# Optimization experiments

Measured on AMD Instinct MI355X. Metric: run time of the kernel, lower is better.

The kernel has to match this reference:

```python
import jax, jax.numpy as jnp
import numpy as np

MOLS = 64
ATOMS = 256
N = MOLS * ATOMS
K_GB = 32
K_GNN = 16
HID = 128
OFFSET = 0.009            # GB dielectric offset (nm)
ALPHA, BETA, GAMMA = 1.0, 0.8, 4.85  # OBC2 coefficients
EPS_FACTOR = 138.935456   # Coulomb constant, kJ*nm/(mol*e^2)
PREF = -EPS_FACTOR * (1.0 - 1.0 / 78.5)


def _edges(key, k_neigh):
    # random intra-molecule neighbors, no self loops (mimics radius-graph structure)
    src = jnp.repeat(jnp.arange(N), k_neigh)
    off = jax.random.randint(key, (N * k_neigh,), 1, ATOMS)
    dst = (src // ATOMS) * ATOMS + (src % ATOMS + off) % ATOMS
    return jnp.stack([src, dst]).astype(jnp.int32)


def setup_inputs() -> dict:
    key = jax.random.key(0)
    ks = jax.random.split(key, 8)
    pos = (jax.random.uniform(ks[0], (N, 3), jnp.float32) * 1.5)
    q = jax.random.uniform(ks[1], (N, 1), jnp.float32) - 0.5
    rad = 0.15 + 0.05 * jax.random.uniform(ks[2], (N, 1), jnp.float32)
    scl = 0.8 + 0.2 * jax.random.uniform(ks[3], (N, 1), jnp.float32)
    rest = jax.random.uniform(ks[4], (N, 4), jnp.float32)
    atom_features = jnp.concatenate([q, rad, scl, rest], axis=1)
    batch = jnp.repeat(jnp.arange(MOLS), ATOMS).astype(jnp.int32)
    edge_index = _edges(ks[5], K_GB)
    gnn_edge_index = _edges(ks[6], K_GNN)

    def lin(k, fi, fo):
        return (jax.random.normal(k, (fi, fo), jnp.float32) / np.float32(np.sqrt(fi)),
                jnp.zeros((fo,), jnp.float32))
    kw = jax.random.split(ks[7], 6)
    i1_w1, i1_b1 = lin(kw[0], 2 * 2 + 1, HID)
    i1_w2, i1_b2 = lin(kw[1], HID, HID)
    i2_w1, i2_b1 = lin(kw[2], 2 * HID + 1, HID)
    i2_w2, i2_b2 = lin(kw[3], HID, HID)
    i3_w1, i3_b1 = lin(kw[4], 2 * HID + 1, HID)
    i3_w2, i3_b2 = lin(kw[5], HID, 1)
    return dict(pos=pos, atom_features=atom_features, batch=batch,
                edge_index=edge_index, gnn_edge_index=gnn_edge_index,
                i1_w1=i1_w1, i1_b1=i1_b1, i1_w2=i1_w2, i1_b2=i1_b2,
                i2_w1=i2_w1, i2_b1=i2_b1, i2_w2=i2_w2, i2_b2=i2_b2,
                i3_w1=i3_w1, i3_b1=i3_b1, i3_w2=i3_w2, i3_b2=i3_b2)


def _dist(pos, ei):
    d2 = jnp.sum((pos[ei[0]] - pos[ei[1]]) ** 2, axis=1)
    return jnp.sqrt(d2 + 1e-12)


def _gb_energies(pos, feats, ei):
    # GBNeck_interaction (Born radii via HCT descreening integral, OBC2 rescale)
    # followed by GBNeck_energies (pairwise GB + self energy), per-atom [N,1]
    n = pos.shape[0]
    src, dst = ei[0], ei[1]
    d = _dist(pos, ei)
    q, radius, scale = feats[:, 0], feats[:, 1], feats[:, 2]
    rho = radius - OFFSET
    sr_j = (scale * rho)[src]
    rho_i = rho[dst]
    U = d + sr_j
    L = jnp.maximum(rho_i, jnp.abs(d - sr_j))
    I = 0.5 * (1.0 / L - 1.0 / U
               + 0.25 * (d - sr_j ** 2 / d) * (1.0 / U ** 2 - 1.0 / L ** 2)
               + 0.5 * jnp.log(L / U) / d)
    I = jnp.where(rho_i < U, I, 0.0)
    Isum = jax.ops.segment_sum(I, dst, num_segments=n)
    psi = Isum * rho
    B = 1.0 / (1.0 / rho - jnp.tanh(ALPHA * psi - BETA * psi ** 2 + GAMMA * psi ** 3) / radius)
    Bi, Bj = B[dst], B[src]
    f_gb = jnp.sqrt(d ** 2 + Bi * Bj * jnp.exp(-d ** 2 / (4.0 * Bi * Bj)))
    e_pair = 0.5 * PREF * q[dst] * q[src] / f_gb  # 0.5: edges are double counted
    e = 0.5 * PREF * q ** 2 / B + jax.ops.segment_sum(e_pair, dst, num_segments=n)
    return e[:, None]


def _in_layer(x, ei, d, w1, b1, w2, b2):
    # IN_layer_all_swish_2pass: edge MLP on [x_i || x_j || d] + scatter-add
    n = x.shape[0]
    m = jnp.concatenate([x[ei[0]], x[ei[1]], d[:, None]], axis=1)
    h = jax.nn.silu(m @ w1 + b1)
    return jax.ops.segment_sum(h @ w2 + b2, ei[1], num_segments=n)


def _energies_all(pos, feats, ei, gei,
                  i1_w1, i1_b1, i1_w2, i1_b2,
                  i2_w1, i2_b1, i2_w2, i2_b2,
                  i3_w1, i3_b1, i3_w2, i3_b2):
    e_gb = _gb_energies(pos, feats, ei)
    d_gnn = _dist(pos, gei)
    x = jax.nn.silu(_in_layer(feats[:, :2], gei, d_gnn, i1_w1, i1_b1, i1_w2, i1_b2))
    x = jax.nn.silu(_in_layer(x, gei, d_gnn, i2_w1, i2_b1, i2_w2, i2_b2))
    x = _in_layer(x, gei, d_gnn, i3_w1, i3_b1, i3_w2, i3_b2)
    return e_gb + x


def reference(pos, atom_features, batch, edge_index, gnn_edge_index,
              i1_w1, i1_b1, i1_w2, i1_b2,
              i2_w1, i2_b1, i2_w2, i2_b2,
              i3_w1, i3_b1, i3_w2, i3_b2):
    ws = (i1_w1, i1_b1, i1_w2, i1_b2, i2_w1, i2_b1, i2_w2, i2_b2,
          i3_w1, i3_b1, i3_w2, i3_b2)
    efun = lambda p: _energies_all(p, atom_features, edge_index, gnn_edge_index, *ws)
    energies, vjp = jax.vjp(efun, pos)  # [N,1]
    (gpos,) = vjp(jnp.ones_like(energies))
    forces = -gpos
    energy = jax.ops.segment_sum(energies[:, 0], batch, num_segments=MOLS)[:, None]
    return energy, forces
```

## Files before the change

kernel.cpp:

```cpp
#include <hip/hip_runtime.h>
#include <hip/hip_bf16.h>

#define NATOMS 16384
#define MOLS   64
#define ATOMSM 256
#define EGB    524288
#define EGNN   262144
#define HID    128
#define NH     (NATOMS*HID)

#define OFFSETC 0.009f
#define ALPHAC  1.0f
#define BETAC   0.8f
#define GAMMAC  4.85f
#define PREFC   (-138.935456f*(1.0f-1.0f/78.5f))

typedef __hip_bfloat16 bf;
typedef __attribute__((ext_vector_type(8))) short bf8v;
typedef __attribute__((ext_vector_type(4))) float f4v;
typedef unsigned int uint;

__device__ __forceinline__ float b2f(bf x){ return __bfloat162float(x); }
__device__ __forceinline__ bf f2b(float x){ return __float2bfloat16(x); }
__device__ __forceinline__ short f2s(float x){ bf h = f2b(x); return *(short*)&h; }
// ... 53 lines not shown
    short* __restrict__ A3at, short* __restrict__ A3bt,
    short* __restrict__ rA2a, short* __restrict__ rA2b,
    short* __restrict__ rA3a, short* __restrict__ rA3b,
    short* __restrict__ rC1, short* __restrict__ rC2,
    const float* __restrict__ feat, const float* __restrict__ A1,
    bf* __restrict__ u1, bf* __restrict__ v1,
    const float* __restrict__ pos, const int* __restrict__ ei,
    float* __restrict__ Isum,
    const int* __restrict__ gei, float* __restrict__ dgnn, int* __restrict__ cnt)
{
    int tid = threadIdx.x;
    if (blockIdx.x < 64){
        int gid = blockIdx.x*256 + tid;
        int j = gid >> 7, k = gid & 127;
        C1t[gid]  = f2s(C1[k*HID+j]);
        C2t[gid]  = f2s(C2[k*HID+j]);
        A2at[gid] = f2s(A2[k*HID+j]);
        A2bt[gid] = f2s(A2[(HID+k)*HID+j]);
        A3at[gid] = f2s(A3[k*HID+j]);
        A3bt[gid] = f2s(A3[(HID+k)*HID+j]);
        rA2a[gid] = f2s(A2[gid]);
        rA2b[gid] = f2s(A2[HID*HID+gid]);
        rA3a[gid] = f2s(A3[gid]);
        rA3b[gid] = f2s(A3[HID*HID+gid]);
        rC1[gid]  = f2s(C1[gid]);
        rC2[gid]  = f2s(C2[gid]);
    } else if (blockIdx.x < 4160){
        int gid2 = (blockIdx.x-64)*256 + tid;
        int i = gid2 >> 6, k2 = (gid2 & 63)*2;
        float q = feat[7*i+0], r = feat[7*i+1];
        float u0 = q*A1[k2]         + r*A1[HID+k2];
        float u1v= q*A1[k2+1]       + r*A1[HID+k2+1];
        float v0 = q*A1[2*HID+k2]   + r*A1[3*HID+k2];
        float v1v= q*A1[2*HID+k2+1] + r*A1[3*HID+k2+1];
        ushort2 uu, vv;
        uu.x = (unsigned short)f2s(u0); uu.y = (unsigned short)f2s(u1v);
        vv.x = (unsigned short)f2s(v0); vv.y = (unsigned short)f2s(v1v);
        *(ushort2*)((short*)u1 + (size_t)i*HID + k2) = uu;
        *(ushort2*)((short*)v1 + (size_t)i*HID + k2) = vv;
    } else if (blockIdx.x < 4672){
        __shared__ float sPx[256], sPy[256], sPz[256], sRho[256], sSr[256];
        __shared__ float sI[256];
        int bb = blockIdx.x - 4160;
        int mbase = (bb >> 3) * 256;
        {
            int i = mbase + tid;
            sPx[tid]=pos[3*i]; sPy[tid]=pos[3*i+1]; sPz[tid]=pos[3*i+2];
            float rad = feat[7*i+1], sc = feat[7*i+2];
            float rho = rad - OFFSETC;
            sRho[tid]=rho; sSr[tid]=sc*rho;
            sI[tid]=0.f;
        }
        __syncthreads();
        int T = bb*256 + tid;
        int s = T >> 3, p = T & 7;
        int sl = s & 255;
        int e0 = s*32 + p*4;
        float px = sPx[sl], py = sPy[sl], pz = sPz[sl];
        float sr = sSr[sl];
        float srr = sr*sr;
        const int* dP = ei + EGB;
        int4 d4 = *(const int4*)(dP + e0);
        int dls[4] = {d4.x&255, d4.y&255, d4.z&255, d4.w&255};
#pragma unroll
        for (int j=0;j<4;j++){
            int dl = dls[j];
            float dx = px - sPx[dl];
            float dy = py - sPy[dl];
            float dz = pz - sPz[dl];
            float d2 = dx*dx+dy*dy+dz*dz + 1e-12f;
            float rd = frsq(d2);
            float d  = d2*rd;
            float rho_i = sRho[dl];
            float U = d + sr;
            if (rho_i < U){
                float L = fmaxf(rho_i, fabsf(d - sr));
                float invU = frcp(U), invL = frcp(L);
                float I = 0.5f*invL - 0.5f*invU
                        + 0.125f*(d - srr*rd)*(invU*invU - invL*invL)
                        + 0.25f*__logf(L*invU)*rd;
                atomicAdd(&sI[dl], I);
            }
        }
        __syncthreads();
        atomicAdd(&Isum[mbase + tid], sI[tid]);
    } else {
        int e = (blockIdx.x-4672)*256 + tid;
        int s = gei[e], dd = gei[EGNN+e];
        float dx = pos[3*s+0] - pos[3*dd+0];
        float dy = pos[3*s+1] - pos[3*dd+1];
        float dz = pos[3*s+2] - pos[3*dd+2];
        dgnn[e] = fsqrt(dx*dx+dy*dy+dz*dz + 1e-12f);
        atomicAdd(&cnt[dd], 1);
    }
}

__global__ __launch_bounds__(256) void k_B(
    const float* __restrict__ feat, const float* __restrict__ Isum,
    float* __restrict__ Bv, float* __restrict__ cB, float* __restrict__ gB,
    float* __restrict__ egb,
    const int* __restrict__ cnt, int* __restrict__ rptr,
    const int* __restrict__ gei, const float* __restrict__ dgnn,
    int* __restrict__ csr, int2* __restrict__ csr2)
{
    int t = threadIdx.x;
    if (blockIdx.x < 64){
        int i = blockIdx.x*256 + t;
        float q   = feat[7*i+0];
        float rad = feat[7*i+1];
        float rho = rad - OFFSETC;
        float psi = Isum[i]*rho;
        float u = psi*(ALPHAC + psi*(-BETAC + GAMMAC*psi));
        float tt = tanhf(u);
        float rrad = frcp(rad);
        float B = frcp(frcp(rho) - tt*rrad);
        Bv[i] = B;
        float du = ALPHAC + psi*(-2.0f*BETAC + 3.0f*GAMMAC*psi);
        cB[i] = B*B*((1.0f-tt*tt)*rrad)*du*rho;
        float Cs = 0.5f*PREFC*q*q;
        float rB = frcp(B);
        egb[i] = Cs*rB;
        gB[i]  = -Cs*rB*rB;
    } else {
        __shared__ int sc[256];
        __shared__ int lcur[256];
        int m = blockIdx.x - 64;
        int c = cnt[m*256+t];
        sc[t] = c; __syncthreads();
        for (int off=1; off<256; off<<=1){
            int x = (t>=off) ? sc[t-off] : 0;
            __syncthreads();
            sc[t] += x;
            __syncthreads();
        }
        int exl = sc[t] - c;
        rptr[m*256+t] = m*4096 + exl;
        lcur[t] = exl;
        __syncthreads();
        int e0 = m*4096;
        for (int j=t; j<4096; j+=256){
            int e = e0 + j;
            int dl = gei[EGNN+e] & 255;
            float d = dgnn[e];
            int p = atomicAdd(&lcur[dl], 1);
            int idx = e0 + p;
            csr[idx] = e;
            int2 rec; rec.x = (e >> 4) << 8;
            rec.y = __float_as_int(d);
            csr2[idx] = rec;
        }
    }
}

__global__ __launch_bounds__(256) void k_gbC(
    const float* __restrict__ pos, const float* __restrict__ feat,
    const int* __restrict__ ei, const float* __restrict__ Bv,
    float* __restrict__ egb, float* __restrict__ gdgb, float* __restrict__ gB)
{
    __shared__ float sPx[256], sPy[256], sPz[256], sB[256], sQf[256];
    __shared__ float sE[256], sG[256];
    int tid = threadIdx.x;
    int mbase = (blockIdx.x >> 3) * 256;
    {
        int i = mbase + tid;
        sPx[tid]=pos[3*i]; sPy[tid]=pos[3*i+1]; sPz[tid]=pos[3*i+2];
        sB[tid]=Bv[i]; sQf[tid]=feat[7*i+0];
        sE[tid]=0.f; sG[tid]=0.f;
    }
    __syncthreads();
    int T = blockIdx.x*256 + tid;
    int s = T >> 3, p = T & 7;
    int sl = s & 255;
    int e0 = s*32 + p*4;
    float px = sPx[sl], py = sPy[sl], pz = sPz[sl];
    float qs = sQf[sl];
    float Bs = sB[sl];
    float gsrc = 0.f;
    const int* dP = ei + EGB;
    int4 d4 = *(const int4*)(dP + e0);
    int dls[4] = {d4.x&255, d4.y&255, d4.z&255, d4.w&255};
#pragma unroll
    for (int j=0;j<4;j++){
        int dl = dls[j];
        float dx = px - sPx[dl];
        float dy = py - sPy[dl];
        float dz = pz - sPz[dl];
        float d2 = dx*dx+dy*dy+dz*dz + 1e-12f;
        float d  = d2*frsq(d2);
        float Bd = sB[dl];
        float C = 0.5f*PREFC*sQf[dl]*qs;
        float P = Bd*Bs;
        float qq = 0.25f*d2*frcp(P);
        float ex = __expf(-qq);
        float f2 = d2 + P*ex;
        float rf = frsq(f2);
        float f3i = rf*rf*rf;
        gdgb[e0+j] = -C*d*(1.f - 0.25f*ex)*f3i;
        float common = -C*ex*(1.f + qq)*0.5f*f3i;
        atomicAdd(&sE[dl], C*rf);
        atomicAdd(&sG[dl], common*Bs);
        gsrc += common*Bd;
    }
    gsrc += __shfl_xor(gsrc,1);
    gsrc += __shfl_xor(gsrc,2);
    gsrc += __shfl_xor(gsrc,4);
    if (p==0) atomicAdd(&sG[sl], gsrc);
    __syncthreads();
    atomicAdd(&egb[mbase + tid], sE[tid]);
    atomicAdd(&gB[mbase + tid],  sG[tid]);
}

__global__ __launch_bounds__(256) void k_gbE(
    const float* __restrict__ pos, const float* __restrict__ feat,
    const int* __restrict__ ei, const float* __restrict__ cB,
    const float* __restrict__ gB,
    const float* __restrict__ gdgb, float* __restrict__ grad)
{
    __shared__ float sPx[256], sPy[256], sPz[256], sRho[256], sSr[256], sCg[256];
    __shared__ float sGx[256], sGy[256], sGz[256];
    int tid = threadIdx.x;
    int mbase = (blockIdx.x >> 3) * 256;
    {
        int i = mbase + tid;
        sPx[tid]=pos[3*i]; sPy[tid]=pos[3*i+1]; sPz[tid]=pos[3*i+2];
        float rad = feat[7*i+1], sc = feat[7*i+2];
        float rho = rad - OFFSETC;
        sRho[tid]=rho; sSr[tid]=sc*rho;
        sCg[tid]=cB[i]*gB[i];
        sGx[tid]=0.f; sGy[tid]=0.f; sGz[tid]=0.f;
    }
    __syncthreads();
    int T = blockIdx.x*256 + tid;
    int s = T >> 3, p = T & 7;
    int sl = s & 255;
    int e0 = s*32 + p*4;
    float px = sPx[sl], py = sPy[sl], pz = sPz[sl];
    float sr = sSr[sl];
    float srr = sr*sr;
    float gx=0.f, gy=0.f, gz=0.f;
    const int* dP = ei + EGB;
    int4 d4 = *(const int4*)(dP + e0);
    int dls[4] = {d4.x&255, d4.y&255, d4.z&255, d4.w&255};
#pragma unroll
    for (int j=0;j<4;j++){
        int dl = dls[j];
        float dx = px - sPx[dl];
        float dy = py - sPy[dl];
        float dz = pz - sPz[dl];
        float d2 = dx*dx+dy*dy+dz*dz + 1e-12f;
        float rd = frsq(d2);
        float d  = d2*rd;
        float rd2 = rd*rd;
        float rho_i = sRho[dl];
        float U = d + sr;
        float gd = gdgb[e0+j];
        if (rho_i < U){
            float aa = fabsf(d - sr);
            float L, Lp;
            if (rho_i >= aa){ L = rho_i; Lp = 0.f; }
            else { L = aa; Lp = (d >= sr) ? 1.f : -1.f; }
            float invU = frcp(U), invL = frcp(L);
            float invU2=invU*invU, invL2=invL*invL;
            float dIdd = -0.5f*Lp*invL2 + 0.5f*invU2
                + 0.125f*(1.f + srr*rd2)*(invU2 - invL2)
                + 0.125f*(d - srr*rd)*(2.f*Lp*invL2*invL - 2.f*invU2*invU)
                + 0.25f*((Lp*invL - invU)*rd - __logf(L*invU)*rd2);
            gd += sCg[dl]*dIdd;
        }
        float c = gd*rd;
        gx += c*dx; gy += c*dy; gz += c*dz;
        atomicAdd(&sGx[dl], -c*dx);
        atomicAdd(&sGy[dl], -c*dy);
        atomicAdd(&sGz[dl], -c*dz);
    }
    gx += __shfl_xor(gx,1); gx += __shfl_xor(gx,2); gx += __shfl_xor(gx,4);
    gy += __shfl_xor(gy,1); gy += __shfl_xor(gy,2); gy += __shfl_xor(gy,4);
    gz += __shfl_xor(gz,1); gz += __shfl_xor(gz,2); gz += __shfl_xor(gz,4);
    if (p==0){
        atomicAdd(&sGx[sl], gx);
        atomicAdd(&sGy[sl], gy);
        atomicAdd(&sGz[sl], gz);
    }
    __syncthreads();
    int i = mbase + tid;
    atomicAdd(&grad[3*i+0], sGx[tid]);
    atomicAdd(&grad[3*i+1], sGy[tid]);
    atomicAdd(&grad[3*i+2], sGz[tid]);
}


template<bool WSDS>
__device__ __forceinline__ void edge_fwd_wave(
    int dst, int lane,
    const int2* __restrict__ csr2, const int* __restrict__ rptr, const int* __restrict__ cnt,
    const uint* __restrict__ u, const uint* __restrict__ v,
    const float* __restrict__ wdp, const float* __restrict__ bb,
    uint* __restrict__ Hs, uint* __restrict__ Sds)
{
    int n = cnt[dst], r0 = rptr[dst];
    float2 wd = *(const float2*)&wdp[2*lane];
    float2 b2 = *(const float2*)&bb[2*lane];
    uint vp = v[dst*64 + lane];
    float base0 = lo2f(vp) + b2.x;
    float base1 = hi2f(vp) + b2.y;
    float h0=0.f,h1=0.f,e0a=0.f,e1a=0.f;
    for (int j0=0; j0<n; j0+=64){
        int m = n - j0; if (m > 64) m = 64;
        int rx = 0, ry = 0;
        if (lane < m){ int2 rc = csr2[r0+j0+lane]; rx = rc.x; ry = rc.y; }
#pragma unroll 2
        for (int j=0;j<m;j++){
            int off = __builtin_amdgcn_readlane(rx, j);
            float d  = __uint_as_float((unsigned)__builtin_amdgcn_readlane(ry, j));
            uint up = *(const uint*)((const char*)u + off + 4*lane);
            float a0 = fmaf(d, wd.x, base0 + lo2f(up));
            float a1 = fmaf(d, wd.y, base1 + hi2f(up));
            float s0 = sigf(a0), s1 = sigf(a1);
            float p0 = a0*s0, p1 = a1*s1;
            h0 += p0; h1 += p1;
            if (WSDS){
                e0a = fmaf(s0, 1.f + a0 - p0, e0a);
                e1a = fmaf(s1, 1.f + a1 - p1, e1a);
            }
        }
    }
    Hs[dst*64+lane] = pack2(h0,h1);
    if (WSDS) Sds[dst*64+lane] = pack2(e0a,e1a);
}

__global__ __launch_bounds__(256,8) void k_edge_fwd0(
    const int2* __restrict__ csr2, const int* __restrict__ rptr, const int* __restrict__ cnt,
    const uint* __restrict__ u, const uint* __restrict__ v,
    const float* __restrict__ wdp, const float* __restrict__ bb,
    uint* __restrict__ Hs)
{
    int lane = threadIdx.x & 63, wid = threadIdx.x >> 6;
    int dst = blockIdx.x*4 + wid;
    edge_fwd_wave<false>(dst, lane, csr2, rptr, cnt, u, v, wdp, bb, Hs, nullptr);
}

__global__ __launch_bounds__(256,8) void k_edge_fwd1(
    const int2* __restrict__ csr2, const int* __restrict__ rptr, const int* __restrict__ cnt,
    const uint* __restrict__ u, const uint* __restrict__ v,
    const float* __restrict__ wdp, const float* __restrict__ bb,
    uint* __restrict__ Hs, uint* __restrict__ Sds)
{
    int lane = threadIdx.x & 63, wid = threadIdx.x >> 6;
    int dst = blockIdx.x*4 + wid;
    edge_fwd_wave<true>(dst, lane, csr2, rptr, cnt, u, v, wdp, bb, Hs, Sds);
}

__global__ __launch_bounds__(256,4) void k_l3(
    const int2* __restrict__ csr2, const int* __restrict__ rptr, const int* __restrict__ cnt,
    const int* __restrict__ gei, const float* __restrict__ dgnn,
    const uint* __restrict__ u, const uint* __restrict__ v,
    const float* __restrict__ A3, const float* __restrict__ B3,
    const float* __restrict__ C3, const float* __restrict__ D3,
    uint* __restrict__ Gd, float* __restrict__ x3,
    uint* __restrict__ Gs, float* __restrict__ gdg)
{
    int lane = threadIdx.x & 63, wid = threadIdx.x >> 6;
    const float* wdp = A3 + 256*HID;
    if (blockIdx.x < NATOMS/4){
        int dst = blockIdx.x*4 + wid;
        int n = cnt[dst], r0 = rptr[dst];
        float2 wd = *(const float2*)&wdp[2*lane];
        float2 b2 = *(const float2*)&B3[2*lane];
        float2 ck = *(const float2*)&C3[2*lane];
        uint vp = v[dst*64 + lane];
        float base0 = lo2f(vp) + b2.x;
        float base1 = hi2f(vp) + b2.y;
        float h0=0.f,h1=0.f,e0a=0.f,e1a=0.f;
        for (int j0=0; j0<n; j0+=64){
            int m = n - j0; if (m > 64) m = 64;
            int rx = 0, ry = 0;
            if (lane < m){ int2 rc = csr2[r0+j0+lane]; rx = rc.x; ry = rc.y; }
#pragma unroll 2
            for (int j=0;j<m;j++){
                int off = __builtin_amdgcn_readlane(rx, j);
                float d  = __uint_as_float((unsigned)__builtin_amdgcn_readlane(ry, j));
                uint up = *(const uint*)((const char*)u + off + 4*lane);
                float a0 = fmaf(d, wd.x, base0 + lo2f(up));
                float a1 = fmaf(d, wd.y, base1 + hi2f(up));
                float s0 = sigf(a0), s1 = sigf(a1);
                float p0 = a0*s0, p1 = a1*s1;
                h0 += p0; h1 += p1;
                e0a = fmaf(s0, 1.f + a0 - p0, e0a);
                e1a = fmaf(s1, 1.f + a1 - p1, e1a);
            }
        }
        Gd[dst*64+lane] = pack2(ck.x*e0a, ck.y*e1a);
        float px = waveRed(ck.x*h0 + ck.y*h1);
        if (lane==0) x3[dst] = px + (float)n*D3[0];
    } else {
        int s = (blockIdx.x - NATOMS/4)*4 + wid;
        int doff = 0, dbit = 0;
        if (lane < 16){
            doff = gei[EGNN + s*16 + lane] << 8;
            dbit = __float_as_int(dgnn[s*16+lane]);
        }
        float2 wd = *(const float2*)&wdp[2*lane];
        float2 b2 = *(const float2*)&B3[2*lane];
        float2 ck = *(const float2*)&C3[2*lane];
        uint up = u[s*64 + lane];
        float us0 = lo2f(up) + b2.x;
        float us1 = hi2f(up) + b2.y;
        float cw0 = ck.x*wd.x, cw1 = ck.y*wd.y;
        float gs0=0.f, gs1=0.f;
        float A[16];
#pragma unroll
        for (int t=0;t<16;t++){
            int off = __builtin_amdgcn_readlane(doff, t);
            float d = __uint_as_float((unsigned)__builtin_amdgcn_readlane(dbit, t));
            uint vp = *(const uint*)((const char*)v + off + 4*lane);
            float a0 = fmaf(d, wd.x, us0 + lo2f(vp));
            float a1 = fmaf(d, wd.y, us1 + hi2f(vp));
            float s0 = sigf(a0), s1 = sigf(a1);
            float p0 = a0*s0, p1 = a1*s1;
            float dv0 = s0*(1.f + a0 - p0);
            float dv1 = s1*(1.f + a1 - p1);
            gs0 += dv0; gs1 += dv1;
            A[t] = fmaf(dv1, cw1, dv0*cw0);
        }
        Gs[s*64+lane] = pack2(ck.x*gs0, ck.y*gs1);
        float tot = red16(A, lane);
        if (lane < 32 && !(lane & 1)) gdg[s*16 + (lane>>1)] = tot;
    }
}

__global__ __launch_bounds__(256,4) void k_bwd_src(
    const int* __restrict__ gei, const float* __restrict__ dgnn,
    const uint* __restrict__ u, const uint* __restrict__ v,
    const float* __restrict__ wdp, const float* __restrict__ bb,
    const uint* __restrict__ gH,
    uint* __restrict__ Gs, float* __restrict__ gdg)
{
    int lane = threadIdx.x & 63, wid = threadIdx.x >> 6;
    int s = blockIdx.x*4 + wid;
    int doff = 0, dbit = 0;
    if (lane < 16){
        doff = gei[EGNN + s*16 + lane] << 8;
        dbit = __float_as_int(dgnn[s*16+lane]);
    }
    float gold = gdg[s*16 + ((lane>>1)&15)];
    float2 wd = *(const float2*)&wdp[2*lane];
    float2 b2 = *(const float2*)&bb[2*lane];
    uint up = u[s*64 + lane];
    float us0 = lo2f(up) + b2.x;
    float us1 = hi2f(up) + b2.y;
    float gs0=0.f, gs1=0.f;
    float A[16];
#pragma unroll
    for (int t=0;t<16;t++){
        int off = __builtin_amdgcn_readlane(doff, t);
        float d = __uint_as_float((unsigned)__builtin_amdgcn_readlane(dbit, t));
        uint vp = *(const uint*)((const char*)v + off + 4*lane);
        uint gp = *(const uint*)((const char*)gH + off + 4*lane);
        float a0 = fmaf(d, wd.x, us0 + lo2f(vp));
        float a1 = fmaf(d, wd.y, us1 + hi2f(vp));
        float s0 = sigf(a0), s1 = sigf(a1);
        float p0 = a0*s0, p1 = a1*s1;
        float ga0 = s0*(1.f + a0 - p0) * lo2f(gp);
        float ga1 = s1*(1.f + a1 - p1) * hi2f(gp);
        gs0 += ga0; gs1 += ga1;
        A[t] = fmaf(ga1, wd.y, ga0*wd.x);
    }
    if (Gs) Gs[s*64+lane] = pack2(gs0, gs1);
    float tot = red16(A, lane);
    if (lane < 32 && !(lane & 1)) gdg[s*16 + (lane>>1)] = gold + tot;
}

__global__ __launch_bounds__(256) void k_node_fwd_uv_mfma(
    const short* __restrict__ Hs, const int* __restrict__ cnt,
    const short* __restrict__ Ct, const float* __restrict__ D,
    const short* __restrict__ Aat, const short* __restrict__ Abt,
    bf* __restrict__ dsz, bf* __restrict__ u, bf* __restrict__ v)
{
    __shared__ short sx[64*HID];
    int lane = threadIdx.x & 63, w = threadIdx.x >> 6;
    int m0 = blockIdx.x*64 + w*16;
    int ar = lane & 15, kg = lane >> 4;
    bf8v af[4];
#pragma unroll
    for (int s=0;s<4;s++) af[s] = *(const bf8v*)&Hs[(size_t)(m0+ar)*HID + s*32 + kg*8];
    f4v acc[8];
#pragma unroll
    for (int nt=0;nt<8;nt++){
        acc[nt] = (f4v){0.f,0.f,0.f,0.f};
        const short* bp = Ct + (nt*16+ar)*HID + kg*8;
#pragma unroll
        for (int s=0;s<4;s++){
            bf8v bv = *(const bf8v*)(bp + s*32);
            acc[nt] = __builtin_amdgcn_mfma_f32_16x16x32_bf16(af[s], bv, acc[nt], 0,0,0);
        }
    }
    float cn[4];
#pragma unroll
    for (int r=0;r<4;r++) cn[r] = (float)cnt[m0 + kg*4 + r];
#pragma unroll
    for (int nt=0;nt<8;nt++){
        int j = nt*16 + ar;
        float Dj = D[j];
#pragma unroll
        for (int r=0;r<4;r++){
            int m = m0 + kg*4 + r;
            float zv = acc[nt][r] + cn[r]*Dj;
            float sg = sigf(zv);
            dsz[(size_t)m*HID + j] = f2b(sg*(1.f + zv*(1.f - sg)));
            sx[(w*16 + kg*4 + r)*HID + j] = f2s(zv*sg);
        }
    }
    __syncthreads();
#pragma unroll
    for (int s=0;s<4;s++) af[s] = *(const bf8v*)&sx[(w*16+ar)*HID + s*32 + kg*8];
    f4v au[8], av[8];
#pragma unroll
    for (int nt=0;nt<8;nt++){
        au[nt] = (f4v){0.f,0.f,0.f,0.f};
        av[nt] = (f4v){0.f,0.f,0.f,0.f};
        const short* bpa = Aat + (nt*16+ar)*HID + kg*8;
        const short* bpb = Abt + (nt*16+ar)*HID + kg*8;
#pragma unroll
        for (int s=0;s<4;s++){
            bf8v ba = *(const bf8v*)(bpa + s*32);
            bf8v bb = *(const bf8v*)(bpb + s*32);
            au[nt] = __builtin_amdgcn_mfma_f32_16x16x32_bf16(af[s], ba, au[nt], 0,0,0);
            av[nt] = __builtin_amdgcn_mfma_f32_16x16x32_bf16(af[s], bb, av[nt], 0,0,0);
        }
    }
#pragma unroll
    for (int nt=0;nt<8;nt++){
        int j = nt*16 + ar;
#pragma unroll
        for (int r=0;r<4;r++){
            int m = m0 + kg*4 + r;
            u[(size_t)m*HID + j] = f2b(au[nt][r]);
            v[(size_t)m*HID + j] = f2b(av[nt][r]);
        }
    }
}

__global__ __launch_bounds__(256) void k_gx_node_bwd_mfma(
    const short* __restrict__ Gs, const short* __restrict__ Gd,
    const short* __restrict__ gHin, const short* __restrict__ Sds,
    const short* __restrict__ Ra, const short* __restrict__ Rb,
    const bf* __restrict__ dsz, const short* __restrict__ Rc,
    bf* __restrict__ gHout)
{
    __shared__ short st[64*HID];
    int lane = threadIdx.x & 63, w = threadIdx.x >> 6;
    int m0 = blockIdx.x*64 + w*16;
    int ar = lane & 15, kg = lane >> 4;
    bf8v as_[4], ad_[4];
#pragma unroll
    for (int s=0;s<4;s++)
        as_[s] = *(const bf8v*)&Gs[(size_t)(m0+ar)*HID + s*32 + kg*8];
    if (Sds){
#pragma unroll
        for (int s=0;s<4;s++){
            bf8v g = *(const bf8v*)&gHin[(size_t)(m0+ar)*HID + s*32 + kg*8];
            bf8v sd = *(const bf8v*)&Sds[(size_t)(m0+ar)*HID + s*32 + kg*8];
            bf8v r;
#pragma unroll
            for (int i=0;i<8;i++) r[i] = f2s(s2f(g[i])*s2f(sd[i]));
            ad_[s] = r;
        }
    } else {
#pragma unroll
        for (int s=0;s<4;s++)
            ad_[s] = *(const bf8v*)&Gd[(size_t)(m0+ar)*HID + s*32 + kg*8];
    }
    f4v acc[8];
#pragma unroll
    for (int nt=0;nt<8;nt++){
        acc[nt] = (f4v){0.f,0.f,0.f,0.f};
        const short* bpa = Ra + (nt*16+ar)*HID + kg*8;
        const short* bpb = Rb + (nt*16+ar)*HID + kg*8;
#pragma unroll
        for (int s=0;s<4;s++){
            bf8v ba = *(const bf8v*)(bpa + s*32);
            bf8v bb = *(const bf8v*)(bpb + s*32);
            acc[nt] = __builtin_amdgcn_mfma_f32_16x16x32_bf16(as_[s], ba, acc[nt], 0,0,0);
            acc[nt] = __builtin_amdgcn_mfma_f32_16x16x32_bf16(ad_[s], bb, acc[nt], 0,0,0);
        }
    }
#pragma unroll
    for (int nt=0;nt<8;nt++){
        int j = nt*16 + ar;
#pragma unroll
        for (int r=0;r<4;r++){
            int m = m0 + kg*4 + r;
            float t = acc[nt][r] * b2f(dsz[(size_t)m*HID + j]);
            st[(w*16 + kg*4 + r)*HID + j] = f2s(t);
        }
    }
    __syncthreads();
    bf8v af[4];
#pragma unroll
    for (int s=0;s<4;s++) af[s] = *(const bf8v*)&st[(w*16+ar)*HID + s*32 + kg*8];
    f4v a2[8];
#pragma unroll
    for (int nt=0;nt<8;nt++){
        a2[nt] = (f4v){0.f,0.f,0.f,0.f};
        const short* bp = Rc + (nt*16+ar)*HID + kg*8;
#pragma unroll
        for (int s=0;s<4;s++){
            bf8v bc = *(const bf8v*)(bp + s*32);
            a2[nt] = __builtin_amdgcn_mfma_f32_16x16x32_bf16(af[s], bc, a2[nt], 0,0,0);
        }
    }
#pragma unroll
    for (int nt=0;nt<8;nt++){
        int j = nt*16 + ar;
#pragma unroll
        for (int r=0;r<4;r++){
            gHout[(size_t)(m0 + kg*4 + r)*HID + j] = f2b(a2[nt][r]);
        }
    }
}

__global__ __launch_bounds__(256) void k_out(
    const float* __restrict__ pos, const int* __restrict__ gei,
    const int* __restrict__ csr, const int* __restrict__ rptr, const int* __restrict__ cnt,
    const float* __restrict__ dgnn, const float* __restrict__ gdg,
    const float* __restrict__ grad,
    const float* __restrict__ egb, const float* __restrict__ x3,
    float* __restrict__ out)
{
    int tid = threadIdx.x;
    if (blockIdx.x < 512){
        float* fout = out + MOLS;
        int T = blockIdx.x*256 + tid;
        int i = T >> 3, p = T & 7;
        float px = pos[3*i+0], py = pos[3*i+1], pz = pos[3*i+2];
        float ax=0.f, ay=0.f, az=0.f;
        for (int j=p;j<16;j+=8){
            int e = i*16 + j;
            int o = gei[EGNN+e];
            float c = gdg[e]*frcp(dgnn[e]);
            ax += c*(px - pos[3*o+0]);
            ay += c*(py - pos[3*o+1]);
            az += c*(pz - pos[3*o+2]);
        }
        int n = cnt[i], r0 = rptr[i];
        for (int j=p;j<n;j+=8){
            int e = csr[r0+j];
            int o = e >> 4;
            float c = gdg[e]*frcp(dgnn[e]);
            ax += c*(px - pos[3*o+0]);
            ay += c*(py - pos[3*o+1]);
            az += c*(pz - pos[3*o+2]);
        }
        ax += __shfl_xor(ax,1); ax += __shfl_xor(ax,2); ax += __shfl_xor(ax,4);
        ay += __shfl_xor(ay,1); ay += __shfl_xor(ay,2); ay += __shfl_xor(ay,4);
        az += __shfl_xor(az,1); az += __shfl_xor(az,2); az += __shfl_xor(az,4);
        if (p==0){
            fout[3*i+0] = -(grad[3*i+0] + ax);
            fout[3*i+1] = -(grad[3*i+1] + ay);
            fout[3*i+2] = -(grad[3*i+2] + az);
        }
    } else {
        __shared__ float red[4];
        int m = blockIdx.x - 512;
        int i = m*ATOMSM + tid;
        float en = egb[i] + x3[i];
        float v = waveRed(en);
        int wave = tid>>6, lane = tid&63;
        if (lane==0) red[wave] = v;
        __syncthreads();
        if (tid==0) out[m] = red[0]+red[1]+red[2]+red[3];
    }
}

extern "C" void kernel_launch(void* const* d_in, const int* in_sizes, int n_in,
                              void* d_out, int out_size, void* d_ws, size_t ws_size,
                              hipStream_t stream)
{
    const float* pos  = (const float*)d_in[0];
    const float* feat = (const float*)d_in[1];
    const int* ei  = (const int*)d_in[3];
    const int* gei = (const int*)d_in[4];
    const float* A1f = (const float*)d_in[5];  const float* B1f = (const float*)d_in[6];
    const float* C1f = (const float*)d_in[7];  const float* D1f = (const float*)d_in[8];
    const float* A2f = (const float*)d_in[9];  const float* B2f = (const float*)d_in[10];
    const float* C2f = (const float*)d_in[11]; const float* D2f = (const float*)d_in[12];
    const float* A3f = (const float*)d_in[13]; const float* B3f = (const float*)d_in[14];
    const float* C3f = (const float*)d_in[15]; const float* D3f = (const float*)d_in[16];

    float* w = (float*)d_ws;
    size_t off = 0;
    auto nxt = [&](size_t n)->float*{ float* p = w + off; off += (n + 255) & ~(size_t)255; return p; };
    float* Isum = nxt(NATOMS);
    int*   cnt  = (int*)nxt(NATOMS);
    float* grad = nxt(3*NATOMS);
    float* Bv = nxt(NATOMS); float* cB = nxt(NATOMS);
    float* gB = nxt(NATOMS); float* egb = nxt(NATOMS); float* x3 = nxt(NATOMS);
    int*   rptr = (int*)nxt(NATOMS);
    int*   csr  = (int*)nxt(EGNN);
    int2*  csr2 = (int2*)nxt((size_t)EGNN*2);
    float* dgnn = nxt(EGNN); float* gdgnn = nxt(EGNN); float* gdgb = nxt(EGB);
    bf* dsz1 = (bf*)nxt(NH/2); bf* dsz2 = (bf*)nxt(NH/2);
    bf* Hs1 = (bf*)nxt(NH/2); bf* Hs2 = (bf*)nxt(NH/2);
    bf* Gs3 = (bf*)nxt(NH/2); bf* Gd3 = (bf*)nxt(NH/2);
    bf* Sds2 = (bf*)nxt(NH/2);
    bf* u1 = (bf*)nxt(NH/2); bf* v1 = (bf*)nxt(NH/2);
    bf* u2 = (bf*)nxt(NH/2); bf* v2 = (bf*)nxt(NH/2);
    bf* v3 = (bf*)nxt(NH/2);
    short* C1t  = (short*)nxt(8192); short* C2t  = (short*)nxt(8192);
    short* A2at = (short*)nxt(8192); short* A2bt = (short*)nxt(8192);
    short* A3at = (short*)nxt(8192); short* A3bt = (short*)nxt(8192);
    short* rA2a = (short*)nxt(8192); short* rA2b = (short*)nxt(8192);
    short* rA3a = (short*)nxt(8192); short* rA3b = (short*)nxt(8192);
    short* rC1  = (short*)nxt(8192); short* rC2  = (short*)nxt(8192);
    bf* u3  = Hs1;
    bf* gH2 = Hs2;
    bf* Gs2 = Gs3;
    bf* gH1 = u3;

    hipMemsetAsync(Isum, 0, (size_t)5*NATOMS*sizeof(float), stream);

    k_A<<<64 + NH/512 + 512 + EGNN/256, 256, 0, stream>>>(
        A2f, C1f, A3f, C2f,
        C1t, C2t, A2at, A2bt, A3at, A3bt, rA2a, rA2b, rA3a, rA3b, rC1, rC2,
        feat, A1f, u1, v1,
        pos, ei, Isum, gei, dgnn, cnt);

    k_B<<<128,256,0,stream>>>(feat, Isum, Bv, cB, gB, egb, cnt, rptr,
                              gei, dgnn, csr, csr2);

    k_edge_fwd0<<<NATOMS/4,256,0,stream>>>(csr2, rptr, cnt, (const uint*)u1, (const uint*)v1,
                                           A1f+4*HID, B1f, (uint*)Hs1);
    k_gbC<<<512,256,0,stream>>>(pos, feat, ei, Bv, egb, gdgb, gB);
    k_node_fwd_uv_mfma<<<NATOMS/64,256,0,stream>>>((const short*)Hs1, cnt, C1t, D1f,
                                                   A2at, A2bt, dsz1, u2, v2);
    k_edge_fwd1<<<NATOMS/4,256,0,stream>>>(csr2, rptr, cnt, (const uint*)u2, (const uint*)v2,
                                           A2f+256*HID, B2f, (uint*)Hs2, (uint*)Sds2);
    k_gbE<<<512,256,0,stream>>>(pos, feat, ei, cB, gB, gdgb, grad);
    k_node_fwd_uv_mfma<<<NATOMS/64,256,0,stream>>>((const short*)Hs2, cnt, C2t, D2f,
                                                   A3at, A3bt, dsz2, u3, v3);

    k_l3<<<2*(NATOMS/4),256,0,stream>>>(csr2, rptr, cnt, gei, dgnn,
                                        (const uint*)u3, (const uint*)v3,
                                        A3f, B3f, C3f, D3f,
                                        (uint*)Gd3, x3, (uint*)Gs3, gdgnn);

    k_gx_node_bwd_mfma<<<NATOMS/64,256,0,stream>>>((const short*)Gs3, (const short*)Gd3,
        (const short*)nullptr, (const short*)nullptr, rA3a, rA3b, dsz2, rC2, gH2);
    k_bwd_src<<<NATOMS/4,256,0,stream>>>(gei, dgnn, (const uint*)u2, (const uint*)v2,
                                         A2f+256*HID, B2f, (const uint*)gH2,
                                         (uint*)Gs2, gdgnn);
    k_gx_node_bwd_mfma<<<NATOMS/64,256,0,stream>>>((const short*)Gs2, (const short*)nullptr,
        (const short*)gH2, (const short*)Sds2, rA2a, rA2b, dsz1, rC1, gH1);
    k_bwd_src<<<NATOMS/4,256,0,stream>>>(gei, dgnn, (const uint*)u1, (const uint*)v1,
                                         A1f+4*HID, B1f, (const uint*)gH1,
                                         (uint*)nullptr, gdgnn);

    k_out<<<576,256,0,stream>>>(pos, gei, csr, rptr, cnt, dgnn, gdgnn,
                                grad, egb, x3, (float*)d_out);
}
```

Baseline: 328.9 us.

## Merge GB kernels into GNN forward launches as independent block ranges

The GB energy kernel (gbC) now shares a launch with the first edge-forward pass, and the GB gradient kernel (gbE) shares a launch with the first node MLP. Block index decides which body a block runs. This cuts two launches and lets independent work fill the GPU together. The gbE body reuses the node kernel's shared buffer to fit shared memory. Separately, the edge gather loops unroll by 4 instead of 2 with a hoisted per-lane base pointer. Risks: merged kernels take the worse register and LDS footprint and launch bounds of the two bodies, and gbE now runs before edge_fwd1 rather than after. That reorder looks safe since gbE depends only on gB, cB and gdgb.

```diff
diff --git a/kernel.cpp b/kernel.cpp
--- a/kernel.cpp
+++ b/kernel.cpp
@@ -229,143 +229,6 @@
     }
 }
 
-__global__ __launch_bounds__(256) void k_gbC(
-    const float* __restrict__ pos, const float* __restrict__ feat,
-    const int* __restrict__ ei, const float* __restrict__ Bv,
-    float* __restrict__ egb, float* __restrict__ gdgb, float* __restrict__ gB)
-{
-    __shared__ float sPx[256], sPy[256], sPz[256], sB[256], sQf[256];
-    __shared__ float sE[256], sG[256];
-    int tid = threadIdx.x;
-    int mbase = (blockIdx.x >> 3) * 256;
-    {
-        int i = mbase + tid;
-        sPx[tid]=pos[3*i]; sPy[tid]=pos[3*i+1]; sPz[tid]=pos[3*i+2];
-        sB[tid]=Bv[i]; sQf[tid]=feat[7*i+0];
-        sE[tid]=0.f; sG[tid]=0.f;
-    }
-    __syncthreads();
-    int T = blockIdx.x*256 + tid;
-    int s = T >> 3, p = T & 7;
-    int sl = s & 255;
-    int e0 = s*32 + p*4;
-    float px = sPx[sl], py = sPy[sl], pz = sPz[sl];
-    float qs = sQf[sl];
-    float Bs = sB[sl];
-    float gsrc = 0.f;
-    const int* dP = ei + EGB;
-    int4 d4 = *(const int4*)(dP + e0);
-    int dls[4] = {d4.x&255, d4.y&255, d4.z&255, d4.w&255};
-#pragma unroll
-    for (int j=0;j<4;j++){
-        int dl = dls[j];
-        float dx = px - sPx[dl];
-        float dy = py - sPy[dl];
-        float dz = pz - sPz[dl];
-        float d2 = dx*dx+dy*dy+dz*dz + 1e-12f;
-        float d  = d2*frsq(d2);
-        float Bd = sB[dl];
-        float C = 0.5f*PREFC*sQf[dl]*qs;
-        float P = Bd*Bs;
-        float qq = 0.25f*d2*frcp(P);
-        float ex = __expf(-qq);
-        float f2 = d2 + P*ex;
-        float rf = frsq(f2);
-        float f3i = rf*rf*rf;
-        gdgb[e0+j] = -C*d*(1.f - 0.25f*ex)*f3i;
-        float common = -C*ex*(1.f + qq)*0.5f*f3i;
-        atomicAdd(&sE[dl], C*rf);
-        atomicAdd(&sG[dl], common*Bs);
-        gsrc += common*Bd;
-    }
-    gsrc += __shfl_xor(gsrc,1);
-    gsrc += __shfl_xor(gsrc,2);
-    gsrc += __shfl_xor(gsrc,4);
-    if (p==0) atomicAdd(&sG[sl], gsrc);
-    __syncthreads();
-    atomicAdd(&egb[mbase + tid], sE[tid]);
-    atomicAdd(&gB[mbase + tid],  sG[tid]);
-}
-
-__global__ __launch_bounds__(256) void k_gbE(
-    const float* __restrict__ pos, const float* __restrict__ feat,
-    const int* __restrict__ ei, const float* __restrict__ cB,
-    const float* __restrict__ gB,
-    const float* __restrict__ gdgb, float* __restrict__ grad)
-{
-    __shared__ float sPx[256], sPy[256], sPz[256], sRho[256], sSr[256], sCg[256];
-    __shared__ float sGx[256], sGy[256], sGz[256];
-    int tid = threadIdx.x;
-    int mbase = (blockIdx.x >> 3) * 256;
-    {
-        int i = mbase + tid;
-        sPx[tid]=pos[3*i]; sPy[tid]=pos[3*i+1]; sPz[tid]=pos[3*i+2];
-        float rad = feat[7*i+1], sc = feat[7*i+2];
-        float rho = rad - OFFSETC;
-        sRho[tid]=rho; sSr[tid]=sc*rho;
-        sCg[tid]=cB[i]*gB[i];
-        sGx[tid]=0.f; sGy[tid]=0.f; sGz[tid]=0.f;
-    }
-    __syncthreads();
-    int T = blockIdx.x*256 + tid;
-    int s = T >> 3, p = T & 7;
-    int sl = s & 255;
-    int e0 = s*32 + p*4;
-    float px = sPx[sl], py = sPy[sl], pz = sPz[sl];
-    float sr = sSr[sl];
-    float srr = sr*sr;
-    float gx=0.f, gy=0.f, gz=0.f;
-    const int* dP = ei + EGB;
-    int4 d4 = *(const int4*)(dP + e0);
-    int dls[4] = {d4.x&255, d4.y&255, d4.z&255, d4.w&255};
-#pragma unroll
-    for (int j=0;j<4;j++){
-        int dl = dls[j];
-        float dx = px - sPx[dl];
-        float dy = py - sPy[dl];
-        float dz = pz - sPz[dl];
-        float d2 = dx*dx+dy*dy+dz*dz + 1e-12f;
-        float rd = frsq(d2);
-        float d  = d2*rd;
-        float rd2 = rd*rd;
-        float rho_i = sRho[dl];
-        float U = d + sr;
-        float gd = gdgb[e0+j];
-        if (rho_i < U){
-            float aa = fabsf(d - sr);
-            float L, Lp;
-            if (rho_i >= aa){ L = rho_i; Lp = 0.f; }
-            else { L = aa; Lp = (d >= sr) ? 1.f : -1.f; }
-            float invU = frcp(U), invL = frcp(L);
-            float invU2=invU*invU, invL2=invL*invL;
-            float dIdd = -0.5f*Lp*invL2 + 0.5f*invU2
-                + 0.125f*(1.f + srr*rd2)*(invU2 - invL2)
-                + 0.125f*(d - srr*rd)*(2.f*Lp*invL2*invL - 2.f*invU2*invU)
-                + 0.25f*((Lp*invL - invU)*rd - __logf(L*invU)*rd2);
-            gd += sCg[dl]*dIdd;
-        }
-        float c = gd*rd;
-        gx += c*dx; gy += c*dy; gz += c*dz;
-        atomicAdd(&sGx[dl], -c*dx);
-        atomicAdd(&sGy[dl], -c*dy);
-        atomicAdd(&sGz[dl], -c*dz);
-    }
-    gx += __shfl_xor(gx,1); gx += __shfl_xor(gx,2); gx += __shfl_xor(gx,4);
-    gy += __shfl_xor(gy,1); gy += __shfl_xor(gy,2); gy += __shfl_xor(gy,4);
-    gz += __shfl_xor(gz,1); gz += __shfl_xor(gz,2); gz += __shfl_xor(gz,4);
-    if (p==0){
-        atomicAdd(&sGx[sl], gx);
-        atomicAdd(&sGy[sl], gy);
-        atomicAdd(&sGz[sl], gz);
-    }
-    __syncthreads();
-    int i = mbase + tid;
-    atomicAdd(&grad[3*i+0], sGx[tid]);
-    atomicAdd(&grad[3*i+1], sGy[tid]);
-    atomicAdd(&grad[3*i+2], sGz[tid]);
-}
-
-
 template<bool WSDS>
 __device__ __forceinline__ void edge_fwd_wave(
     int dst, int lane,
@@ -380,16 +243,17 @@
     uint vp = v[dst*64 + lane];
     float base0 = lo2f(vp) + b2.x;
     float base1 = hi2f(vp) + b2.y;
+    const char* ub = (const char*)u + 4*lane;
     float h0=0.f,h1=0.f,e0a=0.f,e1a=0.f;
     for (int j0=0; j0<n; j0+=64){
         int m = n - j0; if (m > 64) m = 64;
         int rx = 0, ry = 0;
         if (lane < m){ int2 rc = csr2[r0+j0+lane]; rx = rc.x; ry = rc.y; }
-#pragma unroll 2
+#pragma unroll 4
         for (int j=0;j<m;j++){
             int off = __builtin_amdgcn_readlane(rx, j);
             float d  = __uint_as_float((unsigned)__builtin_amdgcn_readlane(ry, j));
-            uint up = *(const uint*)((const char*)u + off + 4*lane);
+            uint up = *(const uint*)(ub + off);
             float a0 = fmaf(d, wd.x, base0 + lo2f(up));
             float a1 = fmaf(d, wd.y, base1 + hi2f(up));
             float s0 = sigf(a0), s1 = sigf(a1);
@@ -405,15 +269,72 @@
     if (WSDS) Sds[dst*64+lane] = pack2(e0a,e1a);
 }
 
-__global__ __launch_bounds__(256,8) void k_edge_fwd0(
+__global__ __launch_bounds__(256,8) void k_ef0C(
+    const float* __restrict__ pos, const float* __restrict__ feat,
+    const int* __restrict__ ei, const float* __restrict__ Bv,
+    float* __restrict__ egb, float* __restrict__ gdgb, float* __restrict__ gB,
     const int2* __restrict__ csr2, const int* __restrict__ rptr, const int* __restrict__ cnt,
     const uint* __restrict__ u, const uint* __restrict__ v,
     const float* __restrict__ wdp, const float* __restrict__ bb,
     uint* __restrict__ Hs)
 {
-    int lane = threadIdx.x & 63, wid = threadIdx.x >> 6;
-    int dst = blockIdx.x*4 + wid;
-    edge_fwd_wave<false>(dst, lane, csr2, rptr, cnt, u, v, wdp, bb, Hs, nullptr);
+    int tid = threadIdx.x;
+    if (blockIdx.x < 512){
+        __shared__ float sPx[256], sPy[256], sPz[256], sB[256], sQf[256];
+        __shared__ float sE[256], sG[256];
+        int mbase = (blockIdx.x >> 3) * 256;
+        {
+            int i = mbase + tid;
+            sPx[tid]=pos[3*i]; sPy[tid]=pos[3*i+1]; sPz[tid]=pos[3*i+2];
+            sB[tid]=Bv[i]; sQf[tid]=feat[7*i+0];
+            sE[tid]=0.f; sG[tid]=0.f;
+        }
+        __syncthreads();
+        int T = blockIdx.x*256 + tid;
+        int s = T >> 3, p = T & 7;
+        int sl = s & 255;
+        int e0 = s*32 + p*4;
+        float px = sPx[sl], py = sPy[sl], pz = sPz[sl];
+        float qs = sQf[sl];
+        float Bs = sB[sl];
+        float gsrc = 0.f;
+        const int* dP = ei + EGB;
+        int4 d4 = *(const int4*)(dP + e0);
+        int dls[4] = {d4.x&255, d4.y&255, d4.z&255, d4.w&255};
+#pragma unroll
+        for (int j=0;j<4;j++){
+            int dl = dls[j];
+            float dx = px - sPx[dl];
+            float dy = py - sPy[dl];
+            float dz = pz - sPz[dl];
+            float d2 = dx*dx+dy*dy+dz*dz + 1e-12f;
+            float d  = d2*frsq(d2);
+            float Bd = sB[dl];
+            float C = 0.5f*PREFC*sQf[dl]*qs;
+            float P = Bd*Bs;
+            float qq = 0.25f*d2*frcp(P);
+            float ex = __expf(-qq);
+            float f2 = d2 + P*ex;
+            float rf = frsq(f2);
+            float f3i = rf*rf*rf;
+            gdgb[e0+j] = -C*d*(1.f - 0.25f*ex)*f3i;
+            float common = -C*ex*(1.f + qq)*0.5f*f3i;
+            atomicAdd(&sE[dl], C*rf);
+            atomicAdd(&sG[dl], common*Bs);
+            gsrc += common*Bd;
+        }
+        gsrc += __shfl_xor(gsrc,1);
+        gsrc += __shfl_xor(gsrc,2);
+        gsrc += __shfl_xor(gsrc,4);
+        if (p==0) atomicAdd(&sG[sl], gsrc);
+        __syncthreads();
+        atomicAdd(&egb[mbase + tid], sE[tid]);
+        atomicAdd(&gB[mbase + tid],  sG[tid]);
+    } else {
+        int lane = tid & 63, wid = tid >> 6;
+        int dst = (blockIdx.x-512)*4 + wid;
+        edge_fwd_wave<false>(dst, lane, csr2, rptr, cnt, u, v, wdp, bb, Hs, nullptr);
+    }
 }
 
 __global__ __launch_bounds__(256,8) void k_edge_fwd1(
@@ -425,6 +346,179 @@
     int lane = threadIdx.x & 63, wid = threadIdx.x >> 6;
     int dst = blockIdx.x*4 + wid;
     edge_fwd_wave<true>(dst, lane, csr2, rptr, cnt, u, v, wdp, bb, Hs, Sds);
+}
+
+__device__ __forceinline__ void node_fwd_body(
+    int blk, int tid,
+    const short* __restrict__ Hs, const int* __restrict__ cnt,
+    const short* __restrict__ Ct, const float* __restrict__ D,
+    const short* __restrict__ Aat, const short* __restrict__ Abt,
+    bf* __restrict__ dsz, bf* __restrict__ u, bf* __restrict__ v,
+    short* sx)
+{
+    int lane = tid & 63, w = tid >> 6;
+    int m0 = blk*64 + w*16;
+    int ar = lane & 15, kg = lane >> 4;
+    bf8v af[4];
+#pragma unroll
+    for (int s=0;s<4;s++) af[s] = *(const bf8v*)&Hs[(size_t)(m0+ar)*HID + s*32 + kg*8];
+    f4v acc[8];
+#pragma unroll
+    for (int nt=0;nt<8;nt++){
+        acc[nt] = (f4v){0.f,0.f,0.f,0.f};
+        const short* bp = Ct + (nt*16+ar)*HID + kg*8;
+#pragma unroll
+        for (int s=0;s<4;s++){
+            bf8v bv = *(const bf8v*)(bp + s*32);
+            acc[nt] = __builtin_amdgcn_mfma_f32_16x16x32_bf16(af[s], bv, acc[nt], 0,0,0);
+        }
+    }
+    float cn[4];
+#pragma unroll
+    for (int r=0;r<4;r++) cn[r] = (float)cnt[m0 + kg*4 + r];
+#pragma unroll
+    for (int nt=0;nt<8;nt++){
+        int j = nt*16 + ar;
+        float Dj = D[j];
+#pragma unroll
+        for (int r=0;r<4;r++){
+            int m = m0 + kg*4 + r;
+            float zv = acc[nt][r] + cn[r]*Dj;
+            float sg = sigf(zv);
+            dsz[(size_t)m*HID + j] = f2b(sg*(1.f + zv*(1.f - sg)));
+            sx[(w*16 + kg*4 + r)*HID + j] = f2s(zv*sg);
+        }
+    }
+    __syncthreads();
+#pragma unroll
+    for (int s=0;s<4;s++) af[s] = *(const bf8v*)&sx[(w*16+ar)*HID + s*32 + kg*8];
+    f4v au[8], av[8];
+#pragma unroll
+    for (int nt=0;nt<8;nt++){
+        au[nt] = (f4v){0.f,0.f,0.f,0.f};
+        av[nt] = (f4v){0.f,0.f,0.f,0.f};
+        const short* bpa = Aat + (nt*16+ar)*HID + kg*8;
+        const short* bpb = Abt + (nt*16+ar)*HID + kg*8;
+#pragma unroll
+        for (int s=0;s<4;s++){
+            bf8v ba = *(const bf8v*)(bpa + s*32);
+            bf8v bb = *(const bf8v*)(bpb + s*32);
+            au[nt] = __builtin_amdgcn_mfma_f32_16x16x32_bf16(af[s], ba, au[nt], 0,0,0);
+            av[nt] = __builtin_amdgcn_mfma_f32_16x16x32_bf16(af[s], bb, av[nt], 0,0,0);
+        }
+    }
+#pragma unroll
+    for (int nt=0;nt<8;nt++){
+        int j = nt*16 + ar;
+#pragma unroll
+        for (int r=0;r<4;r++){
+            int m = m0 + kg*4 + r;
+            u[(size_t)m*HID + j] = f2b(au[nt][r]);
+            v[(size_t)m*HID + j] = f2b(av[nt][r]);
+        }
+    }
+}
+
+__global__ __launch_bounds__(256,4) void k_nf1E(
+    const float* __restrict__ pos, const float* __restrict__ feat,
+    const int* __restrict__ ei, const float* __restrict__ cB,
+    const float* __restrict__ gB,
+    const float* __restrict__ gdgb, float* __restrict__ grad,
+    const short* __restrict__ Hs, const int* __restrict__ cnt,
+    const short* __restrict__ Ct, const float* __restrict__ D,
+    const short* __restrict__ Aat, const short* __restrict__ Abt,
+    bf* __restrict__ dsz, bf* __restrict__ u, bf* __restrict__ v)
+{
+    __shared__ short sx[64*HID];
+    int tid = threadIdx.x;
+    if (blockIdx.x < 512){
+        float* sPx = (float*)sx;
+        float* sPy = sPx + 256;
+        float* sPz = sPy + 256;
+        float* sRho = sPz + 256;
+        float* sSr = sRho + 256;
+        float* sCg = sSr + 256;
+        __shared__ float sGx[256], sGy[256], sGz[256];
+        int mbase = (blockIdx.x >> 3) * 256;
+        {
+            int i = mbase + tid;
+            sPx[tid]=pos[3*i]; sPy[tid]=pos[3*i+1]; sPz[tid]=pos[3*i+2];
+            float rad = feat[7*i+1], sc = feat[7*i+2];
+            float rho = rad - OFFSETC;
+            sRho[tid]=rho; sSr[tid]=sc*rho;
+            sCg[tid]=cB[i]*gB[i];
+            sGx[tid]=0.f; sGy[tid]=0.f; sGz[tid]=0.f;
+        }
+        __syncthreads();
+        int T = blockIdx.x*256 + tid;
+        int s = T >> 3, p = T & 7;
+        int sl = s & 255;
+        int e0 = s*32 + p*4;
+        float px = sPx[sl], py = sPy[sl], pz = sPz[sl];
+        float sr = sSr[sl];
+        float srr = sr*sr;
+        float gx=0.f, gy=0.f, gz=0.f;
+        const int* dP = ei + EGB;
+        int4 d4 = *(const int4*)(dP + e0);
+        int dls[4] = {d4.x&255, d4.y&255, d4.z&255, d4.w&255};
+#pragma unroll
+        for (int j=0;j<4;j++){
+            int dl = dls[j];
+            float dx = px - sPx[dl];
+            float dy = py - sPy[dl];
+            float dz = pz - sPz[dl];
+            float d2 = dx*dx+dy*dy+dz*dz + 1e-12f;
+            float rd = frsq(d2);
+            float d  = d2*rd;
+            float rd2 = rd*rd;
+            float rho_i = sRho[dl];
+            float U = d + sr;
+            float gd = gdgb[e0+j];
+            if (rho_i < U){
+                float aa = fabsf(d - sr);
+                float L, Lp;
+                if (rho_i >= aa){ L = rho_i; Lp = 0.f; }
+                else { L = aa; Lp = (d >= sr) ? 1.f : -1.f; }
+                float invU = frcp(U), invL = frcp(L);
+                float invU2=invU*invU, invL2=invL*invL;
+                float dIdd = -0.5f*Lp*invL2 + 0.5f*invU2
+                    + 0.125f*(1.f + srr*rd2)*(invU2 - invL2)
+                    + 0.125f*(d - srr*rd)*(2.f*Lp*invL2*invL - 2.f*invU2*invU)
+                    + 0.25f*((Lp*invL - invU)*rd - __logf(L*invU)*rd2);
+                gd += sCg[dl]*dIdd;
+            }
+            float c = gd*rd;
+            gx += c*dx; gy += c*dy; gz += c*dz;
+            atomicAdd(&sGx[dl], -c*dx);
+            atomicAdd(&sGy[dl], -c*dy);
+            atomicAdd(&sGz[dl], -c*dz);
+        }
+        gx += __shfl_xor(gx,1); gx += __shfl_xor(gx,2); gx += __shfl_xor(gx,4);
+        gy += __shfl_xor(gy,1); gy += __shfl_xor(gy,2); gy += __shfl_xor(gy,4);
+        gz += __shfl_xor(gz,1); gz += __shfl_xor(gz,2); gz += __shfl_xor(gz,4);
+        if (p==0){
+            atomicAdd(&sGx[sl], gx);
+            atomicAdd(&sGy[sl], gy);
+            atomicAdd(&sGz[sl], gz);
+        }
+        __syncthreads();
+        int i = mbase + tid;
+        atomicAdd(&grad[3*i+0], sGx[tid]);
+        atomicAdd(&grad[3*i+1], sGy[tid]);
+        atomicAdd(&grad[3*i+2], sGz[tid]);
+    } else {
+        node_fwd_body(blockIdx.x-512, tid, Hs, cnt, Ct, D, Aat, Abt, dsz, u, v, sx);
+    }
+}
+
+__global__ __launch_bounds__(256) void k_node_fwd_uv_mfma(
+    const short* __restrict__ Hs, const int* __restrict__ cnt,
+    const short* __restrict__ Ct, const float* __restrict__ D,
+    const short* __restrict__ Aat, const short* __restrict__ Abt,
+    bf* __restrict__ dsz, bf* __restrict__ u, bf* __restrict__ v)
+{
+    __shared__ short sx[64*HID];
+    node_fwd_body(blockIdx.x, threadIdx.x, Hs, cnt, Ct, D, Aat, Abt, dsz, u, v, sx);
 }
 
 __global__ __launch_bounds__(256,4) void k_l3(
@@ -447,16 +541,17 @@
         uint vp = v[dst*64 + lane];
         float base0 = lo2f(vp) + b2.x;
         float base1 = hi2f(vp) + b2.y;
+        const char* ub = (const char*)u + 4*lane;
         float h0=0.f,h1=0.f,e0a=0.f,e1a=0.f;
         for (int j0=0; j0<n; j0+=64){
             int m = n - j0; if (m > 64) m = 64;
             int rx = 0, ry = 0;
             if (lane < m){ int2 rc = csr2[r0+j0+lane]; rx = rc.x; ry = rc.y; }
-#pragma unroll 2
+#pragma unroll 4
             for (int j=0;j<m;j++){
                 int off = __builtin_amdgcn_readlane(rx, j);
                 float d  = __uint_as_float((unsigned)__builtin_amdgcn_readlane(ry, j));
-                uint up = *(const uint*)((const char*)u + off + 4*lane);
+                uint up = *(const uint*)(ub + off);
                 float a0 = fmaf(d, wd.x, base0 + lo2f(up));
                 float a1 = fmaf(d, wd.y, base1 + hi2f(up));
                 float s0 = sigf(a0), s1 = sigf(a1);
@@ -545,76 +640,6 @@
     if (Gs) Gs[s*64+lane] = pack2(gs0, gs1);
     float tot = red16(A, lane);
     if (lane < 32 && !(lane & 1)) gdg[s*16 + (lane>>1)] = gold + tot;
-}
-
-__global__ __launch_bounds__(256) void k_node_fwd_uv_mfma(
-    const short* __restrict__ Hs, const int* __restrict__ cnt,
-    const short* __restrict__ Ct, const float* __restrict__ D,
-    const short* __restrict__ Aat, const short* __restrict__ Abt,
-    bf* __restrict__ dsz, bf* __restrict__ u, bf* __restrict__ v)
-{
-    __shared__ short sx[64*HID];
-    int lane = threadIdx.x & 63, w = threadIdx.x >> 6;
-    int m0 = blockIdx.x*64 + w*16;
-    int ar = lane & 15, kg = lane >> 4;
-    bf8v af[4];
-#pragma unroll
-    for (int s=0;s<4;s++) af[s] = *(const bf8v*)&Hs[(size_t)(m0+ar)*HID + s*32 + kg*8];
-    f4v acc[8];
-#pragma unroll
-    for (int nt=0;nt<8;nt++){
-        acc[nt] = (f4v){0.f,0.f,0.f,0.f};
-        const short* bp = Ct + (nt*16+ar)*HID + kg*8;
-#pragma unroll
-        for (int s=0;s<4;s++){
-            bf8v bv = *(const bf8v*)(bp + s*32);
-            acc[nt] = __builtin_amdgcn_mfma_f32_16x16x32_bf16(af[s], bv, acc[nt], 0,0,0);
-        }
-    }
-    float cn[4];
-#pragma unroll
-    for (int r=0;r<4;r++) cn[r] = (float)cnt[m0 + kg*4 + r];
-#pragma unroll
-    for (int nt=0;nt<8;nt++){
-        int j = nt*16 + ar;
-        float Dj = D[j];
-#pragma unroll
-        for (int r=0;r<4;r++){
-            int m = m0 + kg*4 + r;
-            float zv = acc[nt][r] + cn[r]*Dj;
-            float sg = sigf(zv);
-            dsz[(size_t)m*HID + j] = f2b(sg*(1.f + zv*(1.f - sg)));
-            sx[(w*16 + kg*4 + r)*HID + j] = f2s(zv*sg);
-        }
-    }
-    __syncthreads();
-#pragma unroll
-    for (int s=0;s<4;s++) af[s] = *(const bf8v*)&sx[(w*16+ar)*HID + s*32 + kg*8];
-    f4v au[8], av[8];
-#pragma unroll
-    for (int nt=0;nt<8;nt++){
-        au[nt] = (f4v){0.f,0.f,0.f,0.f};
-        av[nt] = (f4v){0.f,0.f,0.f,0.f};
-        const short* bpa = Aat + (nt*16+ar)*HID + kg*8;
-        const short* bpb = Abt + (nt*16+ar)*HID + kg*8;
-#pragma unroll
-        for (int s=0;s<4;s++){
-            bf8v ba = *(const bf8v*)(bpa + s*32);
-            bf8v bb = *(const bf8v*)(bpb + s*32);
-            au[nt] = __builtin_amdgcn_mfma_f32_16x16x32_bf16(af[s], ba, au[nt], 0,0,0);
-            av[nt] = __builtin_amdgcn_mfma_f32_16x16x32_bf16(af[s], bb, av[nt], 0,0,0);
-        }
-    }
-#pragma unroll
-    for (int nt=0;nt<8;nt++){
-        int j = nt*16 + ar;
-#pragma unroll
-        for (int r=0;r<4;r++){
-            int m = m0 + kg*4 + r;
-            u[(size_t)m*HID + j] = f2b(au[nt][r]);
-            v[(size_t)m*HID + j] = f2b(av[nt][r]);
-        }
-    }
 }
 
 __global__ __launch_bounds__(256) void k_gx_node_bwd_mfma(
@@ -805,14 +830,16 @@
     k_B<<<128,256,0,stream>>>(feat, Isum, Bv, cB, gB, egb, cnt, rptr,
                               gei, dgnn, csr, csr2);
 
-    k_edge_fwd0<<<NATOMS/4,256,0,stream>>>(csr2, rptr, cnt, (const uint*)u1, (const uint*)v1,
-                                           A1f+4*HID, B1f, (uint*)Hs1);
-    k_gbC<<<512,256,0,stream>>>(pos, feat, ei, Bv, egb, gdgb, gB);
-    k_node_fwd_uv_mfma<<<NATOMS/64,256,0,stream>>>((const short*)Hs1, cnt, C1t, D1f,
-                                                   A2at, A2bt, dsz1, u2, v2);
+    k_ef0C<<<512 + NATOMS/4, 256, 0, stream>>>(
+        pos, feat, ei, Bv, egb, gdgb, gB,
+        csr2, rptr, cnt, (const uint*)u1, (const uint*)v1, A1f+4*HID, B1f, (uint*)Hs1);
+
+    k_nf1E<<<512 + NATOMS/64, 256, 0, stream>>>(
+        pos, feat, ei, cB, gB, gdgb, grad,
+        (const short*)Hs1, cnt, C1t, D1f, A2at, A2bt, dsz1, u2, v2);
+
     k_edge_fwd1<<<NATOMS/4,256,0,stream>>>(csr2, rptr, cnt, (const uint*)u2, (const uint*)v2,
                                            A2f+256*HID, B2f, (uint*)Hs2, (uint*)Sds2);
-    k_gbE<<<512,256,0,stream>>>(pos, feat, ei, cB, gB, gdgb, grad);
     k_node_fwd_uv_mfma<<<NATOMS/64,256,0,stream>>>((const short*)Hs2, cnt, C2t, D2f,
                                                    A3at, A3bt, dsz2, u3, v3);
 
```

Result: faster. 310.9 us (-5.5%).
